# Optimization experiments

Measured on AMD Instinct MI355X. Metric: run time of the kernel, lower is better.

The kernel has to match this reference:

```python
import jax, jax.numpy as jnp
import numpy as np

EMBED_DIM = 1024
NUM_HEADS = 16
HEAD_DIM = EMBED_DIM // NUM_HEADS


def setup_inputs() -> dict:
    key = jax.random.key(0)
    ks = jax.random.split(key, 9)
    s = 1.0 / np.sqrt(EMBED_DIM)
    mk = lambda k: jax.random.uniform(k, (EMBED_DIM, EMBED_DIM), jnp.float32, -s, s)
    bk = lambda k: jax.random.uniform(k, (EMBED_DIM,), jnp.float32, -s, s)
    return {
        "input_tensor": jax.random.normal(ks[0], (4, 2048, EMBED_DIM), jnp.float32),
        "wq": mk(ks[1]), "bq": bk(ks[2]),
        "wk": mk(ks[3]), "bk_": bk(ks[4]),
        "wv": mk(ks[5]), "bv": bk(ks[6]),
        "wo": mk(ks[7]), "bo": bk(ks[8]),
    }


def reference(input_tensor, wq, bq, wk, bk_, wv, bv, wo, bo):
    B, S, E = input_tensor.shape
    H, D = NUM_HEADS, HEAD_DIM
    # torch Linear: y = x @ W.T + b
    q = input_tensor @ wq.T + bq
    k = input_tensor @ wk.T + bk_
    v = input_tensor @ wv.T + bv
    q = q.reshape(B, S, H, D).transpose(0, 2, 1, 3)  # [B,H,S,D]
    k = k.reshape(B, S, H, D).transpose(0, 2, 1, 3)
    v = v.reshape(B, S, H, D).transpose(0, 2, 1, 3)
    scores = jnp.einsum('bhsd,bhtd->bhst', q, k) / jnp.sqrt(jnp.float32(D))
    attn = jax.nn.softmax(scores, axis=-1)  # dropout p=0 -> identity
    out = jnp.einsum('bhst,bhtd->bhsd', attn, v)
    out = out.transpose(0, 2, 1, 3).reshape(B, S, E)
    return out @ wo.T + bo
```

## Files before the change

kernel.cpp:

```cpp
#include <hip/hip_runtime.h>

typedef __bf16 bf16x8 __attribute__((ext_vector_type(8)));
typedef float  f32x4  __attribute__((ext_vector_type(4)));
typedef float  f32x16 __attribute__((ext_vector_type(16)));
typedef unsigned u32x4 __attribute__((ext_vector_type(4)));

#define NB 4
#define SEQ 2048
#define EMB 1024
#define NH 16
#define HD 64
#define MTOT (NB * SEQ)

__device__ __forceinline__ unsigned short f2bf(float f) {
    unsigned u = __float_as_uint(f);
    return (unsigned short)((u + 0x7fffu + ((u >> 16) & 1u)) >> 16);
}

__device__ __forceinline__ void gload16(const void* g, void* l) {
    __builtin_amdgcn_global_load_lds(
        (const __attribute__((address_space(1))) unsigned int*)g,
        (__attribute__((address_space(3))) unsigned int*)l,
        16, 0, 0);
}

__global__ __launch_bounds__(256) void cast_f32_bf16(
    const float* __restrict__ src, unsigned short* __restrict__ dst, int n4) {
    int i = blockIdx.x * 256 + threadIdx.x;
    if (i < n4) {
        float4 v = ((const float4*)src)[i];
        ushort4 r;
        r.x = f2bf(v.x); r.y = f2bf(v.y); r.z = f2bf(v.z); r.w = f2bf(v.w);
        ((ushort4*)dst)[i] = r;
    }
}

__global__ __launch_bounds__(256) void cast4_f32_bf16(
    const float* __restrict__ a, const float* __restrict__ b,
    const float* __restrict__ c, const float* __restrict__ d,
    unsigned short* __restrict__ oa, unsigned short* __restrict__ ob,
    unsigned short* __restrict__ oc, unsigned short* __restrict__ od) {
    int which = blockIdx.x >> 10;
    int i = (blockIdx.x & 1023) * 256 + threadIdx.x;
    const float* src = which == 0 ? a : which == 1 ? b : which == 2 ? c : d;
    unsigned short* dst = which == 0 ? oa : which == 1 ? ob : which == 2 ? oc : od;
    float4 v = ((const float4*)src)[i];
    ushort4 r;
    r.x = f2bf(v.x); r.y = f2bf(v.y); r.z = f2bf(v.z); r.w = f2bf(v.w);
    ((ushort4*)dst)[i] = r;
}

__global__ __launch_bounds__(256) void gemm_qkv(
    const unsigned short* __restrict__ A, const unsigned short* __restrict__ W3,
    const float* __restrict__ bq, const float* __restrict__ bk,
    const float* __restrict__ bv, unsigned short* __restrict__ Qo,
    unsigned short* __restrict__ Ko, unsigned short* __restrict__ Vto) {
    constexpr int K = EMB;
    __shared__ __align__(16) unsigned short As[128 * 64];
    __shared__ __align__(16) unsigned short Bs[128 * 64];

    const int lane = threadIdx.x & 63;
    const int wv   = threadIdx.x >> 6;
    const int wr   = wv >> 1, wc = wv & 1;
    const int f    = blockIdx.x;
    const int w    = (f & 7) * 192 + (f >> 3);
    const int m0   = (w / 24) * 128, n0 = (w % 24) * 128;
    const int proj = n0 >> 10;
    const float* bp = proj == 0 ? bq : proj == 1 ? bk : bv;
    const float oscale = proj == 0 ? 0.18033688011112043f : 1.0f;

    f32x4 acc[4][4];
#pragma unroll
    for (int a = 0; a < 4; ++a)
#pragma unroll
        for (int b = 0; b < 4; ++b) acc[a][b] = (f32x4){0.f, 0.f, 0.f, 0.f};

    const int gsw = ((lane & 7) ^ (lane >> 3)) * 8;
    for (int kt = 0; kt < K / 64; ++kt) {
        if (kt) __syncthreads();
#pragma unroll
        for (int j = 0; j < 4; ++j) {
            int rb = (wv * 4 + j) * 8;
            int r  = rb + (lane >> 3);
            gload16(A + (size_t)(m0 + r) * K + kt * 64 + gsw, &As[rb * 64]);
            gload16(W3 + (size_t)(n0 + r) * K + kt * 64 + gsw, &Bs[rb * 64]);
        }
        __syncthreads();
#pragma unroll
        for (int ks = 0; ks < 2; ++ks) {
            const int slot = ((ks * 4 + (lane >> 4)) ^ (lane & 7)) * 8;
            bf16x8 af[4], bf_[4];
#pragma unroll
            for (int x = 0; x < 4; ++x) {
                af[x]  = *(const bf16x8*)&As[(wr * 64 + x * 16 + (lane & 15)) * 64 + slot];
                bf_[x] = *(const bf16x8*)&Bs[(wc * 64 + x * 16 + (lane & 15)) * 64 + slot];
            }
#pragma unroll
            for (int mi = 0; mi < 4; ++mi)
#pragma unroll
                for (int ni = 0; ni < 4; ++ni)
                    acc[mi][ni] = __builtin_amdgcn_mfma_f32_16x16x32_bf16(
                        af[mi], bf_[ni], acc[mi][ni], 0, 0, 0);
        }
    }

#pragma unroll
    for (int mi = 0; mi < 4; ++mi) {
#pragma unroll
        for (int ni = 0; ni < 4; ++ni) {
            int n    = n0 + wc * 64 + ni * 16 + (lane & 15);
            int nloc = n & 1023;
            float bvv = bp[nloc];
            int h = nloc >> 6, d = nloc & 63;
#pragma unroll
            for (int i = 0; i < 4; ++i) {
                int m = m0 + wr * 64 + mi * 16 + (lane >> 4) * 4 + i;
                float v = (acc[mi][ni][i] + bvv) * oscale;
                int b = m >> 11, s = m & (SEQ - 1);
                if (proj == 0)
                    Qo[(((size_t)(b * NH + h) * SEQ + s) << 6) + d] = f2bf(v);
                else if (proj == 1)
                    Ko[(((size_t)(b * NH + h) * SEQ + s) << 6) + d] = f2bf(v);
                else
                    Vto[((size_t)(b * NH + h) * 64 + d) * SEQ + s] = f2bf(v);
            }
        }
    }
}

__global__ __launch_bounds__(256) void gemm_out(
    const unsigned short* __restrict__ A, const unsigned short* __restrict__ W,
    const float* __restrict__ bias, float* __restrict__ out) {
    constexpr int K = EMB;
    __shared__ __align__(16) unsigned short As[128 * 64];
    __shared__ __align__(16) unsigned short Bs[128 * 64];

    const int lane = threadIdx.x & 63;
    const int wv   = threadIdx.x >> 6;
    const int wr   = wv >> 1, wc = wv & 1;
    const int f    = blockIdx.x;
    const int w    = (f & 7) * 64 + (f >> 3);
    const int m0   = (w / 8) * 128, n0 = (w % 8) * 128;

    f32x4 acc[4][4];
#pragma unroll
    for (int a = 0; a < 4; ++a)
#pragma unroll
        for (int b = 0; b < 4; ++b) acc[a][b] = (f32x4){0.f, 0.f, 0.f, 0.f};

    const int gsw = ((lane & 7) ^ (lane >> 3)) * 8;
    for (int kt = 0; kt < K / 64; ++kt) {
        if (kt) __syncthreads();
#pragma unroll
        for (int j = 0; j < 4; ++j) {
            int rb = (wv * 4 + j) * 8;
            int r  = rb + (lane >> 3);
            gload16(A + (size_t)(m0 + r) * K + kt * 64 + gsw, &As[rb * 64]);
            gload16(W + (size_t)(n0 + r) * K + kt * 64 + gsw, &Bs[rb * 64]);
        }
        __syncthreads();
#pragma unroll
        for (int ks = 0; ks < 2; ++ks) {
            const int slot = ((ks * 4 + (lane >> 4)) ^ (lane & 7)) * 8;
            bf16x8 af[4], bf_[4];
#pragma unroll
            for (int x = 0; x < 4; ++x) {
                af[x]  = *(const bf16x8*)&As[(wr * 64 + x * 16 + (lane & 15)) * 64 + slot];
                bf_[x] = *(const bf16x8*)&Bs[(wc * 64 + x * 16 + (lane & 15)) * 64 + slot];
            }
#pragma unroll
            for (int mi = 0; mi < 4; ++mi)
#pragma unroll
                for (int ni = 0; ni < 4; ++ni)
                    acc[mi][ni] = __builtin_amdgcn_mfma_f32_16x16x32_bf16(
                        af[mi], bf_[ni], acc[mi][ni], 0, 0, 0);
        }
    }

#pragma unroll
    for (int mi = 0; mi < 4; ++mi) {
#pragma unroll
        for (int ni = 0; ni < 4; ++ni) {
            int n = n0 + wc * 64 + ni * 16 + (lane & 15);
            float bv = bias[n];
#pragma unroll
            for (int i = 0; i < 4; ++i) {
                int m = m0 + wr * 64 + mi * 16 + (lane >> 4) * 4 + i;
                out[(size_t)m * EMB + n] = acc[mi][ni][i] + bv;
            }
        }
    }
}

__global__ __launch_bounds__(512, 4) void attn_fwd(
    const unsigned short* __restrict__ Q, const unsigned short* __restrict__ K,
    const unsigned short* __restrict__ Vt, unsigned short* __restrict__ AO) {
    const int qt = blockIdx.x >> 6;
    const int bh = blockIdx.x & 63;
    const int lane = threadIdx.x & 63;
    const int wv   = threadIdx.x >> 6;
    const int l31  = lane & 31;
    const int lh   = lane >> 5;

    __shared__ __align__(16) unsigned short Ks[2][8 * 64 * 8];
    __shared__ __align__(16) unsigned short Vs[2][8 * 64 * 8];

    const unsigned short* Kb = K + (size_t)bh * SEQ * HD;
    const unsigned short* Vb = Vt + (size_t)bh * HD * SEQ;

    const unsigned short* Qp = Q + ((size_t)bh * SEQ + qt * 256 + wv * 32 + l31) * HD + lh * 8;
    bf16x8 qfr[4];
#pragma unroll
    for (int kc = 0; kc < 4; ++kc) qfr[kc] = *(const bf16x8*)(Qp + kc * 16);

    f32x16 oT[2];
#pragma unroll
    for (int r = 0; r < 16; ++r) { oT[0][r] = 0.f; oT[1][r] = 0.f; }
    float lacc = 0.f;

    auto stageKV = [&](int buf, int t) {
        gload16(Kb + (size_t)(t * 64 + lane) * HD + wv * 8, &Ks[buf][wv * 512]);
        gload16(Vb + (size_t)lane * SEQ + t * 64 + wv * 8, &Vs[buf][wv * 512]);
    };

    stageKV(0, 0);

    for (int t = 0; t < SEQ / 64; ++t) {
        const int cur = t & 1;
        __syncthreads();
        if (t + 1 < SEQ / 64) stageKV(cur ^ 1, t + 1);

#pragma unroll
        for (int sub = 0; sub < 2; ++sub) {
            f32x16 st;
#pragma unroll
            for (int r = 0; r < 16; ++r) st[r] = 0.f;
            const int krow = sub * 32 + l31;
            __builtin_amdgcn_s_setprio(1);
#pragma unroll
            for (int kc = 0; kc < 4; ++kc) {
                bf16x8 kf = *(const bf16x8*)&Ks[cur][(kc * 2 + lh) * 512 + krow * 8];
                st = __builtin_amdgcn_mfma_f32_32x32x16_bf16(kf, qfr[kc], st, 0, 0, 0);
            }
            __builtin_amdgcn_s_setprio(0);

            unsigned w0, w1, w2, w3, w4, w5, w6, w7;
#define EXPPK(WI, RA, RB)                                                     \
            {                                                                 \
                float pa = __builtin_amdgcn_exp2f(st[RA]);                    \
                float pb = __builtin_amdgcn_exp2f(st[RB]);                    \
                lacc += pa + pb;                                              \
                asm("v_cvt_pk_bf16_f32 %0, %1, %2" : "=v"(WI) : "v"(pa), "v"(pb)); \
            }
            EXPPK(w0, 0, 1)  EXPPK(w1, 2, 3)  EXPPK(w2, 4, 5)  EXPPK(w3, 6, 7)
            EXPPK(w4, 8, 9)  EXPPK(w5, 10, 11) EXPPK(w6, 12, 13) EXPPK(w7, 14, 15)
#undef EXPPK
            asm volatile("v_permlane32_swap_b32 %0, %1" : "+v"(w0), "+v"(w2));
            asm volatile("v_permlane32_swap_b32 %0, %1" : "+v"(w1), "+v"(w3));
            asm volatile("v_permlane32_swap_b32 %0, %1" : "+v"(w4), "+v"(w6));
            asm volatile("v_permlane32_swap_b32 %0, %1" : "+v"(w5), "+v"(w7));
            u32x4 a0 = {w0, w1, w2, w3};
            u32x4 a1 = {w4, w5, w6, w7};
            bf16x8 pf0 = __builtin_bit_cast(bf16x8, a0);
            bf16x8 pf1 = __builtin_bit_cast(bf16x8, a1);

            __builtin_amdgcn_s_setprio(1);
#pragma unroll
            for (int dt = 0; dt < 2; ++dt) {
                int d = dt * 32 + l31;
#pragma unroll
                for (int ks = 0; ks < 2; ++ks) {
                    bf16x8 vf = *(const bf16x8*)&Vs[cur][(sub * 4 + ks * 2 + lh) * 512 + d * 8];
                    oT[dt] = __builtin_amdgcn_mfma_f32_32x32x16_bf16(
                        vf, ks ? pf1 : pf0, oT[dt], 0, 0, 0);
                }
            }
            __builtin_amdgcn_s_setprio(0);
        }
    }

    float l = lacc + __shfl_xor(lacc, 32);
    float inv = 1.0f / l;
    const int b = bh >> 4, h = bh & 15;
    const int q = qt * 256 + wv * 32 + l31;
    unsigned short* aor = AO + (((size_t)b * SEQ + q) * NH + h) * HD;
#pragma unroll
    for (int dt = 0; dt < 2; ++dt) {
#pragma unroll
        for (int g = 0; g < 4; ++g) {
            ushort4 o;
            o.x = f2bf(oT[dt][g * 4 + 0] * inv);
            o.y = f2bf(oT[dt][g * 4 + 1] * inv);
            o.z = f2bf(oT[dt][g * 4 + 2] * inv);
            o.w = f2bf(oT[dt][g * 4 + 3] * inv);
            *(ushort4*)(aor + dt * 32 + g * 8 + lh * 4) = o;
        }
    }
}

extern "C" void kernel_launch(void* const* d_in, const int* in_sizes, int n_in,
                              void* d_out, int out_size, void* d_ws, size_t ws_size,
                              hipStream_t stream) {
    const float* X  = (const float*)d_in[0];
    const float* wq = (const float*)d_in[1];
    const float* bq = (const float*)d_in[2];
    const float* wk = (const float*)d_in[3];
    const float* bk = (const float*)d_in[4];
    const float* wv = (const float*)d_in[5];
    const float* bv = (const float*)d_in[6];
    const float* wo = (const float*)d_in[7];
    const float* bo = (const float*)d_in[8];
    float* out = (float*)d_out;

    unsigned short* ws = (unsigned short*)d_ws;
    const size_t XE = (size_t)MTOT * EMB;
    const size_t WE = (size_t)EMB * EMB;
    unsigned short* Xb  = ws;
    unsigned short* Wqb = ws + XE;
    unsigned short* Wkb = Wqb + WE;
    unsigned short* Wvb = Wkb + WE;
    unsigned short* Wob = Wvb + WE;
    unsigned short* Qb  = Wob + WE;
    unsigned short* Kb  = Qb + XE;
    unsigned short* Vtb = Kb + XE;
    unsigned short* AOb = Xb;

    cast_f32_bf16<<<(int)(XE / 4 / 256), 256, 0, stream>>>(X, Xb, (int)(XE / 4));
    cast4_f32_bf16<<<4096, 256, 0, stream>>>(wq, wk, wv, wo, Wqb, Wkb, Wvb, Wob);

    gemm_qkv<<<1536, 256, 0, stream>>>(Xb, Wqb, bq, bk, bv, Qb, Kb, Vtb);

    attn_fwd<<<512, 512, 0, stream>>>(Qb, Kb, Vtb, AOb);

    gemm_out<<<512, 256, 0, stream>>>(AOb, Wob, bo, out);
}
```

Before: 184.4 us.

## Fuse input fp32-to-bf16 cast into QKV GEMM and compute softmax sum via MFMA

Removes the standalone cast kernel for the activation tensor. The QKV GEMM now loads fp32 rows directly, converts them to bf16 in registers and writes them swizzled into LDS. Separately, the attention kernel drops the per-lane scalar accumulation of exp values and cross-lane shuffle, and instead computes the row sum with extra MFMAs against a ones vector. The trade-off is that each GEMM tile re-reads fp32 X (24 column tiles per row block, twice the bytes) through synchronous loads instead of async global-to-LDS loads, and each attention step issues two more MFMAs.

```diff
diff --git a/kernel.cpp b/kernel.cpp
--- a/kernel.cpp
+++ b/kernel.cpp
@@ -22,17 +22,6 @@
         (const __attribute__((address_space(1))) unsigned int*)g,
         (__attribute__((address_space(3))) unsigned int*)l,
         16, 0, 0);
-}
-
-__global__ __launch_bounds__(256) void cast_f32_bf16(
-    const float* __restrict__ src, unsigned short* __restrict__ dst, int n4) {
-    int i = blockIdx.x * 256 + threadIdx.x;
-    if (i < n4) {
-        float4 v = ((const float4*)src)[i];
-        ushort4 r;
-        r.x = f2bf(v.x); r.y = f2bf(v.y); r.z = f2bf(v.z); r.w = f2bf(v.w);
-        ((ushort4*)dst)[i] = r;
-    }
 }
 
 __global__ __launch_bounds__(256) void cast4_f32_bf16(
@@ -51,7 +40,7 @@
 }
 
 __global__ __launch_bounds__(256) void gemm_qkv(
-    const unsigned short* __restrict__ A, const unsigned short* __restrict__ W3,
+    const float* __restrict__ Xf, const unsigned short* __restrict__ W3,
     const float* __restrict__ bq, const float* __restrict__ bk,
     const float* __restrict__ bv, unsigned short* __restrict__ Qo,
     unsigned short* __restrict__ Ko, unsigned short* __restrict__ Vto) {
@@ -82,8 +71,22 @@
         for (int j = 0; j < 4; ++j) {
             int rb = (wv * 4 + j) * 8;
             int r  = rb + (lane >> 3);
-            gload16(A + (size_t)(m0 + r) * K + kt * 64 + gsw, &As[rb * 64]);
             gload16(W3 + (size_t)(n0 + r) * K + kt * 64 + gsw, &Bs[rb * 64]);
+        }
+#pragma unroll
+        for (int j = 0; j < 4; ++j) {
+            int gi   = j * 256 + (int)threadIdx.x;
+            int r    = gi >> 3, slot = gi & 7;
+            const float* src = Xf + (size_t)(m0 + r) * K + kt * 64 + ((slot ^ (r & 7)) * 8);
+            float4 v0 = *(const float4*)src;
+            float4 v1 = *(const float4*)(src + 4);
+            unsigned p0, p1, p2, p3;
+            asm("v_cvt_pk_bf16_f32 %0, %1, %2" : "=v"(p0) : "v"(v0.x), "v"(v0.y));
+            asm("v_cvt_pk_bf16_f32 %0, %1, %2" : "=v"(p1) : "v"(v0.z), "v"(v0.w));
+            asm("v_cvt_pk_bf16_f32 %0, %1, %2" : "=v"(p2) : "v"(v1.x), "v"(v1.y));
+            asm("v_cvt_pk_bf16_f32 %0, %1, %2" : "=v"(p3) : "v"(v1.z), "v"(v1.w));
+            u32x4 pk = {p0, p1, p2, p3};
+            *(u32x4*)&As[r * 64 + slot * 8] = pk;
         }
         __syncthreads();
 #pragma unroll
@@ -213,10 +216,12 @@
 #pragma unroll
     for (int kc = 0; kc < 4; ++kc) qfr[kc] = *(const bf16x8*)(Qp + kc * 16);
 
-    f32x16 oT[2];
-#pragma unroll
-    for (int r = 0; r < 16; ++r) { oT[0][r] = 0.f; oT[1][r] = 0.f; }
-    float lacc = 0.f;
+    const u32x4 onesu = {0x3F803F80u, 0x3F803F80u, 0x3F803F80u, 0x3F803F80u};
+    const bf16x8 ones = __builtin_bit_cast(bf16x8, onesu);
+
+    f32x16 oT[2], lT;
+#pragma unroll
+    for (int r = 0; r < 16; ++r) { oT[0][r] = 0.f; oT[1][r] = 0.f; lT[r] = 0.f; }
 
     auto stageKV = [&](int buf, int t) {
         gload16(Kb + (size_t)(t * 64 + lane) * HD + wv * 8, &Ks[buf][wv * 512]);
@@ -249,7 +254,6 @@
             {                                                                 \
                 float pa = __builtin_amdgcn_exp2f(st[RA]);                    \
                 float pb = __builtin_amdgcn_exp2f(st[RB]);                    \
-                lacc += pa + pb;                                              \
                 asm("v_cvt_pk_bf16_f32 %0, %1, %2" : "=v"(WI) : "v"(pa), "v"(pb)); \
             }
             EXPPK(w0, 0, 1)  EXPPK(w1, 2, 3)  EXPPK(w2, 4, 5)  EXPPK(w3, 6, 7)
@@ -265,6 +269,8 @@
             bf16x8 pf1 = __builtin_bit_cast(bf16x8, a1);
 
             __builtin_amdgcn_s_setprio(1);
+            lT = __builtin_amdgcn_mfma_f32_32x32x16_bf16(ones, pf0, lT, 0, 0, 0);
+            lT = __builtin_amdgcn_mfma_f32_32x32x16_bf16(ones, pf1, lT, 0, 0, 0);
 #pragma unroll
             for (int dt = 0; dt < 2; ++dt) {
                 int d = dt * 32 + l31;
@@ -279,8 +285,7 @@
         }
     }
 
-    float l = lacc + __shfl_xor(lacc, 32);
-    float inv = 1.0f / l;
+    float inv = 1.0f / lT[0];
     const int b = bh >> 4, h = bh & 15;
     const int q = qt * 256 + wv * 32 + l31;
     unsigned short* aor = AO + (((size_t)b * SEQ + q) * NH + h) * HD;
@@ -315,7 +320,7 @@
     unsigned short* ws = (unsigned short*)d_ws;
     const size_t XE = (size_t)MTOT * EMB;
     const size_t WE = (size_t)EMB * EMB;
-    unsigned short* Xb  = ws;
+    unsigned short* AOb = ws;
     unsigned short* Wqb = ws + XE;
     unsigned short* Wkb = Wqb + WE;
     unsigned short* Wvb = Wkb + WE;
@@ -323,12 +328,10 @@
     unsigned short* Qb  = Wob + WE;
     unsigned short* Kb  = Qb + XE;
     unsigned short* Vtb = Kb + XE;
-    unsigned short* AOb = Xb;
-
-    cast_f32_bf16<<<(int)(XE / 4 / 256), 256, 0, stream>>>(X, Xb, (int)(XE / 4));
+
     cast4_f32_bf16<<<4096, 256, 0, stream>>>(wq, wk, wv, wo, Wqb, Wkb, Wvb, Wob);
 
-    gemm_qkv<<<1536, 256, 0, stream>>>(Xb, Wqb, bq, bk, bv, Qb, Kb, Vtb);
+    gemm_qkv<<<1536, 256, 0, stream>>>(X, Wqb, bq, bk, bv, Qb, Kb, Vtb);
 
     attn_fwd<<<512, 512, 0, stream>>>(Qb, Kb, Vtb, AOb);
 
```

New measurement: 196.6 us. 6.6% more time.
